# Performance work log

Hardware: AMD Instinct MI355X
Metric: run time of the kernel (lower is better)

The kernel has to match this reference:

```python
import jax, jax.numpy as jnp
import numpy as np

N_NODES = 100000
N_EDGES = 1600000
F_IN = 128
H = 32
N_CLASSES = 2
N_GRAPHS = 1000
BN_EPS = 1e-5


def _glorot(key, shape):
    fan_in, fan_out = shape
    lim = float(np.sqrt(6.0 / (fan_in + fan_out)))
    return jax.random.uniform(key, shape, jnp.float32, -lim, lim)


def setup_inputs() -> dict:
    key = jax.random.key(0)
    ks = jax.random.split(key, 16)
    x = jax.random.normal(ks[0], (N_NODES, F_IN), jnp.float32)
    edge_index = jax.random.randint(ks[1], (2, N_EDGES), 0, N_NODES, jnp.int64)
    batch = jnp.sort(jax.random.randint(ks[2], (N_NODES,), 0, N_GRAPHS, jnp.int64))
    return {
        "x": x,
        "edge_index": edge_index,
        "batch": batch,
        # GIN layer 1 MLP: Linear(F_IN,H) -> BN(H) -> ReLU -> Linear(H,H)
        "W1": _glorot(ks[3], (F_IN, H)), "b1": jnp.zeros((H,), jnp.float32),
        "g1": jnp.ones((H,), jnp.float32), "be1": jnp.zeros((H,), jnp.float32),
        "W2": _glorot(ks[4], (H, H)), "b2": jnp.zeros((H,), jnp.float32),
        # GIN layer 2 MLP
        "W3": _glorot(ks[5], (H, H)), "b3": jnp.zeros((H,), jnp.float32),
        "g2": jnp.ones((H,), jnp.float32), "be2": jnp.zeros((H,), jnp.float32),
        "W4": _glorot(ks[6], (H, H)), "b4": jnp.zeros((H,), jnp.float32),
        # classifier: Linear(2H,H) -> ReLU -> (Dropout eval) -> Linear(H,C)
        "Wc1": _glorot(ks[7], (2 * H, H)), "bc1": jnp.zeros((H,), jnp.float32),
        "Wc2": _glorot(ks[8], (H, N_CLASSES)), "bc2": jnp.zeros((N_CLASSES,), jnp.float32),
    }


def _gin_conv(x, src, dst, W_a, b_a, g, be, W_b, b_b):
    # GIN aggregation with eps=0: (1+eps)*x + sum_{j in N(i)} x_j
    agg = x + jax.ops.segment_sum(x[src], dst, num_segments=N_NODES)
    h = agg @ W_a + b_a                    # [N, H]
    # BatchNorm1d over node dim (training-mode batch stats)
    mu = jnp.mean(h, axis=0)
    var = jnp.var(h, axis=0)
    h = (h - mu) * jax.lax.rsqrt(var + BN_EPS) * g + be
    h = jax.nn.relu(h)
    return h @ W_b + b_b                   # [N, H]


def reference(x, edge_index, batch,
              W1, b1, g1, be1, W2, b2,
              W3, b3, g2, be2, W4, b4,
              Wc1, bc1, Wc2, bc2):
    src, dst = edge_index[0], edge_index[1]
    h = jax.nn.relu(_gin_conv(x, src, dst, W1, b1, g1, be1, W2, b2))
    h = _gin_conv(h, src, dst, W3, b3, g2, be2, W4, b4)   # [N, H]
    # global mean + max pool per graph
    counts = jax.ops.segment_sum(jnp.ones((N_NODES,), h.dtype), batch,
                                 num_segments=N_GRAPHS)              # [G]
    sums = jax.ops.segment_sum(h, batch, num_segments=N_GRAPHS)      # [G, H]
    mean = sums / jnp.maximum(counts, 1.0)[:, None]
    mx = jax.ops.segment_max(h, batch, num_segments=N_GRAPHS)
    mx = jnp.where(counts[:, None] > 0, mx, 0.0)
    z = jnp.concatenate([mean, mx], axis=-1)                          # [G, 2H]
    z = jax.nn.relu(z @ Wc1 + bc1)                                    # dropout: eval mode (identity)
    return z @ Wc2 + bc2                                              # [G, C]
```

## Files before the change

### kernel.cpp

```cpp
#include <hip/hip_runtime.h>


#define H 32
#define FIN 128
#define AGG_BLOCKS 2048
#define BNRED_NB 64

#define BKT_SHIFT 9
#define BKT_SZ 512
#define ACHUNK 4096

__device__ __forceinline__ int lower_bound_i(const int* __restrict__ a, int n, int key) {
  int lo = 0, hi = n;
  while (lo < hi) { int mid = (lo + hi) >> 1; if (a[mid] < key) lo = mid + 1; else hi = mid; }
  return lo;
}


__global__ __launch_bounds__(256) void k_bhist(const int* __restrict__ dst, int E,
                                               int* __restrict__ gbcnt) {
  __shared__ int cnt[256];
  int t = threadIdx.x;
  int e0 = blockIdx.x * ACHUNK, e1 = min(e0 + ACHUNK, E);
  cnt[t] = 0;
  __syncthreads();
  for (int i = e0 + t; i < e1; i += 256) atomicAdd(&cnt[dst[i] >> BKT_SHIFT], 1);
  __syncthreads();
  if (cnt[t] > 0) atomicAdd(&gbcnt[t], cnt[t]);
}

__global__ __launch_bounds__(256) void k_bscan(const int* __restrict__ gbcnt, int nbuck,
                                               int* __restrict__ bbase, int* __restrict__ bcur) {
  int t = threadIdx.x;
  __shared__ int sh[256];
  int v0 = (t < nbuck) ? gbcnt[t] : 0;
  sh[t] = v0;
  __syncthreads();
  for (int d = 1; d < 256; d <<= 1) {
    int v = (t >= d) ? sh[t - d] : 0;
    __syncthreads();
    sh[t] += v;
    __syncthreads();
  }
  int excl = sh[t] - v0;
  if (t < nbuck) { bbase[t] = excl; bcur[t] = excl; }
  if (t == 255) bbase[nbuck] = sh[255];
}

__global__ __launch_bounds__(256) void k_bucketA(const int* __restrict__ src, const int* __restrict__ dst,
                                                 int E, int* __restrict__ bcur,
                                                 unsigned* __restrict__ staging) {
  __shared__ int cnt[256];
  __shared__ int base[256];
  int t = threadIdx.x;
  int e0 = blockIdx.x * ACHUNK, e1 = min(e0 + ACHUNK, E);
  cnt[t] = 0;
  __syncthreads();
  for (int i = e0 + t; i < e1; i += 256) atomicAdd(&cnt[dst[i] >> BKT_SHIFT], 1);
  __syncthreads();
  int c = cnt[t];
  base[t] = (c > 0) ? atomicAdd(&bcur[t], c) : 0;
  __syncthreads();
  for (int i = e0 + t; i < e1; i += 256) {
    int d = dst[i];
    int p = atomicAdd(&base[d >> BKT_SHIFT], 1);
    staging[p] = ((unsigned)(d & (BKT_SZ - 1)) << 17) | (unsigned)src[i];
  }
}

__global__ __launch_bounds__(256) void k_bucketB(const unsigned* __restrict__ staging,
                                                 const int* __restrict__ bbase, int N,
                                                 int* __restrict__ row_ptr, int* __restrict__ csr) {
  __shared__ int cnt[BKT_SZ];
  __shared__ int ptr[BKT_SZ];
  __shared__ int sc[256];
  int t = threadIdx.x, b = blockIdx.x;
  int nb0 = b << BKT_SHIFT;
  int nb1 = min(nb0 + BKT_SZ, N);
  int seg0 = bbase[b];
  int len = bbase[b + 1] - seg0;
  cnt[t] = 0; cnt[t + 256] = 0;
  __syncthreads();
  for (int i = t; i < len; i += 256) atomicAdd(&cnt[staging[seg0 + i] >> 17], 1);
  __syncthreads();
  int s2 = cnt[2 * t] + cnt[2 * t + 1];
  sc[t] = s2;
  __syncthreads();
  for (int d = 1; d < 256; d <<= 1) {
    int v = (t >= d) ? sc[t - d] : 0;
    __syncthreads();
    sc[t] += v;
    __syncthreads();
  }
  int base0 = sc[t] - s2;
  ptr[2 * t] = base0;
  ptr[2 * t + 1] = base0 + cnt[2 * t];
  __syncthreads();
  int nn = nb1 - nb0;
  if (2 * t < nn)     row_ptr[nb0 + 2 * t]     = seg0 + ptr[2 * t];
  if (2 * t + 1 < nn) row_ptr[nb0 + 2 * t + 1] = seg0 + ptr[2 * t + 1];
  if (t == 0 && nb1 == N) row_ptr[N] = seg0 + len;
  __syncthreads();
  for (int i = t; i < len; i += 256) {
    unsigned e = staging[seg0 + i];
    int d = (int)(e >> 17);
    int k = atomicAdd(&ptr[d], 1);
    csr[seg0 + k] = (int)(e & 0x1FFFFu);
  }
}


__global__ __launch_bounds__(256) void k_gemm1(const float* __restrict__ x, const float* __restrict__ W,
                                               float* __restrict__ y, int N) {
  __shared__ __align__(16) float ws[FIN * H];
  __shared__ __align__(16) float xs[128 * 33];
  int t = threadIdx.x;
  for (int i = t; i < FIN * H; i += 256) ws[i] = W[i];
  int nb = blockIdx.x * 128;
  int r0 = (t >> 3) * 4;
  int c0 = (t & 7) * 4;
  float acc[4][4] = {{0.f,0.f,0.f,0.f},{0.f,0.f,0.f,0.f},{0.f,0.f,0.f,0.f},{0.f,0.f,0.f,0.f}};
  for (int kb = 0; kb < FIN; kb += 32) {
    __syncthreads();
    for (int i = t; i < 1024; i += 256) {
      int n = i >> 3, k4 = (i & 7) * 4;
      float4 v = make_float4(0.f, 0.f, 0.f, 0.f);
      int gn = nb + n;
      if (gn < N) v = *(const float4*)&x[(size_t)gn * FIN + kb + k4];
      xs[n * 33 + k4 + 0] = v.x; xs[n * 33 + k4 + 1] = v.y;
      xs[n * 33 + k4 + 2] = v.z; xs[n * 33 + k4 + 3] = v.w;
    }
    __syncthreads();
#pragma unroll
    for (int k = 0; k < 32; ++k) {
      float4 wv = *(const float4*)&ws[(kb + k) * H + c0];
      float x0 = xs[(r0 + 0) * 33 + k];
      float x1 = xs[(r0 + 1) * 33 + k];
      float x2 = xs[(r0 + 2) * 33 + k];
      float x3 = xs[(r0 + 3) * 33 + k];
      acc[0][0] += x0 * wv.x; acc[0][1] += x0 * wv.y; acc[0][2] += x0 * wv.z; acc[0][3] += x0 * wv.w;
      acc[1][0] += x1 * wv.x; acc[1][1] += x1 * wv.y; acc[1][2] += x1 * wv.z; acc[1][3] += x1 * wv.w;
      acc[2][0] += x2 * wv.x; acc[2][1] += x2 * wv.y; acc[2][2] += x2 * wv.z; acc[2][3] += x2 * wv.w;
      acc[3][0] += x3 * wv.x; acc[3][1] += x3 * wv.y; acc[3][2] += x3 * wv.z; acc[3][3] += x3 * wv.w;
    }
  }
#pragma unroll
  for (int r = 0; r < 4; ++r) {
    int gn = nb + r0 + r;
    if (gn < N)
      *(float4*)&y[(size_t)gn * H + c0] = make_float4(acc[r][0], acc[r][1], acc[r][2], acc[r][3]);
  }
}

__global__ __launch_bounds__(256) void k_agg(const float* __restrict__ y, const float* __restrict__ bias,
                                             const int* __restrict__ row_ptr, const int* __restrict__ csr,
                                             float* __restrict__ hout, float* __restrict__ bn_part, int N) {
  int wid = threadIdx.x >> 6, lane = threadIdx.x & 63;
  int c = lane & 31, ep = lane >> 5;
  float rsum = 0.f, rsq = 0.f;
  float bc = bias[c];
  int stride = gridDim.x * 4;
  for (int n = blockIdx.x * 4 + wid; n < N; n += stride) {
    int beg = row_ptr[n], end = row_ptr[n + 1];
    float acc = 0.f;
    for (int b0 = beg; b0 < end; b0 += 64) {
      int m = end - b0; if (m > 64) m = 64;
      int idx = (lane < m) ? csr[b0 + lane] : 0;
      int r = 0;
      for (; r + 8 <= m; r += 8) {
        int j0 = __shfl(idx, r + 0 + ep, 64);
        int j1 = __shfl(idx, r + 2 + ep, 64);
        int j2 = __shfl(idx, r + 4 + ep, 64);
        int j3 = __shfl(idx, r + 6 + ep, 64);
        float v0 = y[(size_t)j0 * H + c];
        float v1 = y[(size_t)j1 * H + c];
        float v2 = y[(size_t)j2 * H + c];
        float v3 = y[(size_t)j3 * H + c];
        acc += (v0 + v1) + (v2 + v3);
      }
      for (; r < m; r += 2) {
        int s = r + ep;
        int j = __shfl(idx, (s < m) ? s : 0, 64);
        float val = y[(size_t)j * H + c];
        if (s < m) acc += val;
      }
    }
    acc += __shfl_xor(acc, 32, 64);
    float v = acc + y[(size_t)n * H + c] + bc;
    if (ep == 0) {
      hout[(size_t)n * H + c] = v;
      rsum += v; rsq += v * v;
    }
  }
  __shared__ float bsum[4][H], bsq[4][H];
  if (ep == 0) { bsum[wid][c] = rsum; bsq[wid][c] = rsq; }
  __syncthreads();
  if (threadIdx.x < H) {
    int cc = threadIdx.x;
    bn_part[(size_t)blockIdx.x * 64 + cc]     = bsum[0][cc] + bsum[1][cc] + bsum[2][cc] + bsum[3][cc];
    bn_part[(size_t)blockIdx.x * 64 + H + cc] = bsq[0][cc] + bsq[1][cc] + bsq[2][cc] + bsq[3][cc];
  }
}

__global__ __launch_bounds__(256) void k_bnred(const float* __restrict__ part,
                                               float* __restrict__ part2) {
  int t = threadIdx.x, b = blockIdx.x;
  int col = t & 63, q = t >> 6;
  int rpb = AGG_BLOCKS / BNRED_NB;
  int r0 = b * rpb + q * (rpb / 4);
  float s = 0.f;
  for (int r = r0; r < r0 + rpb / 4; ++r) s += part[(size_t)r * 64 + col];
  __shared__ float red[4][64];
  red[q][col] = s;
  __syncthreads();
  if (t < 64) part2[(size_t)b * 64 + t] = red[0][t] + red[1][t] + red[2][t] + red[3][t];
}

__global__ __launch_bounds__(256) void k_bnfin(const float* __restrict__ part, int nblk,
                                               const float* __restrict__ gma, const float* __restrict__ bet,
                                               float* __restrict__ sc, float invN) {
  int t = threadIdx.x;
  int col = t & 63, q = t >> 6;
  int per = nblk >> 2;
  float s = 0.f;
  for (int r = q * per; r < (q + 1) * per; ++r) s += part[(size_t)r * 64 + col];
  __shared__ float red[4][64];
  __shared__ float tot[64];
  red[q][col] = s;
  __syncthreads();
  if (t < 64) tot[t] = red[0][t] + red[1][t] + red[2][t] + red[3][t];
  __syncthreads();
  if (t < H) {
    float mean = tot[t] * invN;
    float var = tot[H + t] * invN - mean * mean;
    float scale = gma[t] * rsqrtf(var + 1e-5f);
    sc[t] = scale;
    sc[H + t] = bet[t] - mean * scale;
  }
}

__global__ __launch_bounds__(256) void k_mlp1(const float* __restrict__ h1, const float* __restrict__ sc,
                                              const float* __restrict__ W2, const float* __restrict__ b2,
                                              const float* __restrict__ W3, float* __restrict__ y2, int N) {
  __shared__ __align__(16) float ws2[H * H], ws3[H * H];
  __shared__ __align__(16) float as[128 * 33];
  __shared__ __align__(16) float us[128 * 33];
  __shared__ float scs[2 * H], b2s[H];
  int t = threadIdx.x;
  for (int i = t; i < H * H; i += 256) { ws2[i] = W2[i]; ws3[i] = W3[i]; }
  if (t < 2 * H) scs[t] = sc[t];
  if (t < H) b2s[t] = b2[t];
  __syncthreads();
  int nb = blockIdx.x * 128;
  for (int i = t; i < 1024; i += 256) {
    int n = i >> 3, c4 = (i & 7) * 4;
    int gn = nb + n;
    float4 v = make_float4(0.f, 0.f, 0.f, 0.f);
    if (gn < N) v = *(const float4*)&h1[(size_t)gn * H + c4];
    as[n * 33 + c4 + 0] = fmaxf(v.x * scs[c4 + 0] + scs[H + c4 + 0], 0.f);
    as[n * 33 + c4 + 1] = fmaxf(v.y * scs[c4 + 1] + scs[H + c4 + 1], 0.f);
    as[n * 33 + c4 + 2] = fmaxf(v.z * scs[c4 + 2] + scs[H + c4 + 2], 0.f);
    as[n * 33 + c4 + 3] = fmaxf(v.w * scs[c4 + 3] + scs[H + c4 + 3], 0.f);
  }
  __syncthreads();
  int r0 = (t >> 3) * 4, c0 = (t & 7) * 4;
  float acc[4][4];
#pragma unroll
  for (int i = 0; i < 4; ++i)
#pragma unroll
    for (int j = 0; j < 4; ++j) acc[i][j] = b2s[c0 + j];
#pragma unroll
  for (int k = 0; k < H; ++k) {
    float4 wv = *(const float4*)&ws2[k * H + c0];
    float x0 = as[(r0 + 0) * 33 + k];
    float x1 = as[(r0 + 1) * 33 + k];
    float x2 = as[(r0 + 2) * 33 + k];
    float x3 = as[(r0 + 3) * 33 + k];
    acc[0][0] += x0 * wv.x; acc[0][1] += x0 * wv.y; acc[0][2] += x0 * wv.z; acc[0][3] += x0 * wv.w;
    acc[1][0] += x1 * wv.x; acc[1][1] += x1 * wv.y; acc[1][2] += x1 * wv.z; acc[1][3] += x1 * wv.w;
    acc[2][0] += x2 * wv.x; acc[2][1] += x2 * wv.y; acc[2][2] += x2 * wv.z; acc[2][3] += x2 * wv.w;
    acc[3][0] += x3 * wv.x; acc[3][1] += x3 * wv.y; acc[3][2] += x3 * wv.z; acc[3][3] += x3 * wv.w;
  }
#pragma unroll
  for (int i = 0; i < 4; ++i) {
    us[(r0 + i) * 33 + c0 + 0] = fmaxf(acc[i][0], 0.f);
    us[(r0 + i) * 33 + c0 + 1] = fmaxf(acc[i][1], 0.f);
    us[(r0 + i) * 33 + c0 + 2] = fmaxf(acc[i][2], 0.f);
    us[(r0 + i) * 33 + c0 + 3] = fmaxf(acc[i][3], 0.f);
  }
  __syncthreads();
#pragma unroll
  for (int i = 0; i < 4; ++i)
#pragma unroll
    for (int j = 0; j < 4; ++j) acc[i][j] = 0.f;
#pragma unroll
  for (int k = 0; k < H; ++k) {
    float4 wv = *(const float4*)&ws3[k * H + c0];
    float x0 = us[(r0 + 0) * 33 + k];
    float x1 = us[(r0 + 1) * 33 + k];
    float x2 = us[(r0 + 2) * 33 + k];
    float x3 = us[(r0 + 3) * 33 + k];
    acc[0][0] += x0 * wv.x; acc[0][1] += x0 * wv.y; acc[0][2] += x0 * wv.z; acc[0][3] += x0 * wv.w;
    acc[1][0] += x1 * wv.x; acc[1][1] += x1 * wv.y; acc[1][2] += x1 * wv.z; acc[1][3] += x1 * wv.w;
    acc[2][0] += x2 * wv.x; acc[2][1] += x2 * wv.y; acc[2][2] += x2 * wv.z; acc[2][3] += x2 * wv.w;
    acc[3][0] += x3 * wv.x; acc[3][1] += x3 * wv.y; acc[3][2] += x3 * wv.z; acc[3][3] += x3 * wv.w;
  }
#pragma unroll
  for (int i = 0; i < 4; ++i) {
    int gn = nb + r0 + i;
    if (gn < N)
      *(float4*)&y2[(size_t)gn * H + c0] = make_float4(acc[i][0], acc[i][1], acc[i][2], acc[i][3]);
  }
}

__global__ __launch_bounds__(256) void k_mlp2(const float* __restrict__ hpre, const float* __restrict__ sc,
                                              const float* __restrict__ W4, const float* __restrict__ b4,
                                              float* __restrict__ h2, int N) {
  __shared__ __align__(16) float ws4[H * H];
  __shared__ __align__(16) float as[128 * 33];
  __shared__ float scs[2 * H], b4s[H];
  int t = threadIdx.x;
  for (int i = t; i < H * H; i += 256) ws4[i] = W4[i];
  if (t < 2 * H) scs[t] = sc[t];
  if (t < H) b4s[t] = b4[t];
  __syncthreads();
  int nb = blockIdx.x * 128;
  for (int i = t; i < 1024; i += 256) {
    int n = i >> 3, c4 = (i & 7) * 4;
    int gn = nb + n;
    float4 v = make_float4(0.f, 0.f, 0.f, 0.f);
    if (gn < N) v = *(const float4*)&hpre[(size_t)gn * H + c4];
    as[n * 33 + c4 + 0] = fmaxf(v.x * scs[c4 + 0] + scs[H + c4 + 0], 0.f);
    as[n * 33 + c4 + 1] = fmaxf(v.y * scs[c4 + 1] + scs[H + c4 + 1], 0.f);
    as[n * 33 + c4 + 2] = fmaxf(v.z * scs[c4 + 2] + scs[H + c4 + 2], 0.f);
    as[n * 33 + c4 + 3] = fmaxf(v.w * scs[c4 + 3] + scs[H + c4 + 3], 0.f);
  }
  __syncthreads();
  int r0 = (t >> 3) * 4, c0 = (t & 7) * 4;
  float acc[4][4];
#pragma unroll
  for (int i = 0; i < 4; ++i)
#pragma unroll
    for (int j = 0; j < 4; ++j) acc[i][j] = b4s[c0 + j];
#pragma unroll
  for (int k = 0; k < H; ++k) {
    float4 wv = *(const float4*)&ws4[k * H + c0];
    float x0 = as[(r0 + 0) * 33 + k];
    float x1 = as[(r0 + 1) * 33 + k];
    float x2 = as[(r0 + 2) * 33 + k];
    float x3 = as[(r0 + 3) * 33 + k];
    acc[0][0] += x0 * wv.x; acc[0][1] += x0 * wv.y; acc[0][2] += x0 * wv.z; acc[0][3] += x0 * wv.w;
    acc[1][0] += x1 * wv.x; acc[1][1] += x1 * wv.y; acc[1][2] += x1 * wv.z; acc[1][3] += x1 * wv.w;
    acc[2][0] += x2 * wv.x; acc[2][1] += x2 * wv.y; acc[2][2] += x2 * wv.z; acc[2][3] += x2 * wv.w;
    acc[3][0] += x3 * wv.x; acc[3][1] += x3 * wv.y; acc[3][2] += x3 * wv.z; acc[3][3] += x3 * wv.w;
  }
#pragma unroll
  for (int i = 0; i < 4; ++i) {
    int gn = nb + r0 + i;
    if (gn < N)
      *(float4*)&h2[(size_t)gn * H + c0] = make_float4(acc[i][0], acc[i][1], acc[i][2], acc[i][3]);
  }
}

__global__ __launch_bounds__(256) void k_pool(const float* __restrict__ h2, const int* __restrict__ batch,
                                              int N, int G, float* __restrict__ z) {
  int wid = threadIdx.x >> 6, lane = threadIdx.x & 63;
  int g = blockIdx.x * 4 + wid;
  if (g >= G) return;
  int beg = lower_bound_i(batch, N, g);
  int end = lower_bound_i(batch, N, g + 1);
  int c = lane & 31, ep = lane >> 5;
  float s = 0.f, m = -3.402823466e38f;
  for (int i = beg + ep; i < end; i += 2) {
    float v = h2[(size_t)i * H + c];
    s += v; m = fmaxf(m, v);
  }
  s += __shfl_xor(s, 32, 64);
  m = fmaxf(m, __shfl_xor(m, 32, 64));
  if (ep == 0) {
    int cnt = end - beg;
    z[(size_t)g * 64 + c]     = (cnt > 0) ? s / (float)cnt : 0.f;
    z[(size_t)g * 64 + H + c] = (cnt > 0) ? m : 0.f;
  }
}

__global__ __launch_bounds__(256) void k_cls(const float* __restrict__ z, const float* __restrict__ Wc1,
                                             const float* __restrict__ bc1, const float* __restrict__ Wc2,
                                             const float* __restrict__ bc2, float* __restrict__ out, int G) {
  __shared__ __align__(16) float w1s[64 * H];
  __shared__ float w2s[H * 2], b1s[H], b2s[2];
  int t = threadIdx.x;
  for (int i = t; i < 64 * H; i += 256) w1s[i] = Wc1[i];
  if (t < H * 2) w2s[t] = Wc2[t];
  if (t < H) b1s[t] = bc1[t];
  if (t < 2) b2s[t] = bc2[t];
  __syncthreads();
  int g = blockIdx.x * 256 + t;
  if (g >= G) return;
  float zr[64], u[H];
  const float4* zp = (const float4*)&z[(size_t)g * 64];
#pragma unroll
  for (int q = 0; q < 16; ++q) {
    float4 v = zp[q];
    zr[q * 4 + 0] = v.x; zr[q * 4 + 1] = v.y; zr[q * 4 + 2] = v.z; zr[q * 4 + 3] = v.w;
  }
#pragma unroll
  for (int c = 0; c < H; ++c) u[c] = b1s[c];
#pragma unroll
  for (int k = 0; k < 64; ++k) {
    float av = zr[k];
    const float4* wr = (const float4*)&w1s[k * H];
#pragma unroll
    for (int q = 0; q < H / 4; ++q) {
      float4 wv = wr[q];
      u[q * 4 + 0] += av * wv.x; u[q * 4 + 1] += av * wv.y;
      u[q * 4 + 2] += av * wv.z; u[q * 4 + 3] += av * wv.w;
    }
  }
  float o0 = b2s[0], o1 = b2s[1];
#pragma unroll
  for (int k = 0; k < H; ++k) {
    float uv = fmaxf(u[k], 0.f);
    o0 += uv * w2s[k * 2 + 0];
    o1 += uv * w2s[k * 2 + 1];
  }
  out[(size_t)g * 2 + 0] = o0;
  out[(size_t)g * 2 + 1] = o1;
}

extern "C" void kernel_launch(void* const* d_in, const int* in_sizes, int n_in,
                              void* d_out, int out_size, void* d_ws, size_t ws_size,
                              hipStream_t stream) {
  const float* x    = (const float*)d_in[0];
  const int*   eidx = (const int*)d_in[1];
  const int*   batch= (const int*)d_in[2];
  const float* W1 = (const float*)d_in[3];
  const float* b1 = (const float*)d_in[4];
  const float* g1 = (const float*)d_in[5];
  const float* be1= (const float*)d_in[6];
  const float* W2 = (const float*)d_in[7];
  const float* b2 = (const float*)d_in[8];
  const float* W3 = (const float*)d_in[9];
  const float* b3 = (const float*)d_in[10];
  const float* g2 = (const float*)d_in[11];
  const float* be2= (const float*)d_in[12];
  const float* W4 = (const float*)d_in[13];
  const float* b4 = (const float*)d_in[14];
  const float* Wc1= (const float*)d_in[15];
  const float* bc1= (const float*)d_in[16];
  const float* Wc2= (const float*)d_in[17];
  const float* bc2= (const float*)d_in[18];
  (void)n_in; (void)ws_size;

  int N = in_sizes[2];
  int E = in_sizes[1] / 2;
  int G = out_size / 2;
  int nbuck = (N + BKT_SZ - 1) >> BKT_SHIFT;
  const int* srcv = eidx;
  const int* dstv = eidx + E;

  char* w = (char*)d_ws;
  auto carve = [&](size_t bytes) { void* p = (void*)w; w += (bytes + 255) & ~(size_t)255; return p; };
  float*    bufA    = (float*)carve((size_t)N * H * 4);
  float*    bufB    = (float*)carve((size_t)N * H * 4);
  int*      row_ptr = (int*)carve((size_t)(N + 1) * 4);
  int*      csr     = (int*)carve((size_t)E * 4);
  unsigned* staging = (unsigned*)carve((size_t)E * 4);
  int*      gbcnt   = (int*)carve(256 * 4);
  int*      bbase   = (int*)carve(257 * 4);
  int*      bcur    = (int*)carve(256 * 4);
  float*    bnp     = (float*)carve((size_t)AGG_BLOCKS * 64 * 4);
  float*    bnp2    = (float*)carve((size_t)BNRED_NB * 64 * 4);
  float*    sc1     = (float*)carve(64 * 4);
  float*    sc2     = (float*)carve(64 * 4);
  float*    z       = (float*)carve((size_t)G * 64 * 4);

  int abk = (E + ACHUNK - 1) / ACHUNK;
  int tblk = (N + 127) / 128;

  hipMemsetAsync(gbcnt, 0, 256 * 4, stream);
  k_bhist<<<abk, 256, 0, stream>>>(dstv, E, gbcnt);
  k_bscan<<<1, 256, 0, stream>>>(gbcnt, nbuck, bbase, bcur);
  k_bucketA<<<abk, 256, 0, stream>>>(srcv, dstv, E, bcur, staging);
  k_bucketB<<<nbuck, 256, 0, stream>>>(staging, bbase, N, row_ptr, csr);
  k_gemm1<<<tblk, 256, 0, stream>>>(x, W1, bufA, N);
  k_agg<<<AGG_BLOCKS, 256, 0, stream>>>(bufA, b1, row_ptr, csr, bufB, bnp, N);
  k_bnred<<<BNRED_NB, 256, 0, stream>>>(bnp, bnp2);
  k_bnfin<<<1, 256, 0, stream>>>(bnp2, BNRED_NB, g1, be1, sc1, 1.0f / (float)N);
  k_mlp1<<<tblk, 256, 0, stream>>>(bufB, sc1, W2, b2, W3, bufA, N);
  k_agg<<<AGG_BLOCKS, 256, 0, stream>>>(bufA, b3, row_ptr, csr, bufB, bnp, N);
  k_bnred<<<BNRED_NB, 256, 0, stream>>>(bnp, bnp2);
  k_bnfin<<<1, 256, 0, stream>>>(bnp2, BNRED_NB, g2, be2, sc2, 1.0f / (float)N);
  k_mlp2<<<tblk, 256, 0, stream>>>(bufB, sc2, W4, b4, bufA, N);
  k_pool<<<(G + 3) / 4, 256, 0, stream>>>(bufA, batch, N, G, z);
  k_cls<<<(G + 255) / 256, 256, 0, stream>>>(z, Wc1, bc1, Wc2, bc2, (float*)d_out, G);
}
```

Before: 389.6 us.

## Double-buffer x tiles in gemm1 with register prefetch and smaller row tiles

Rewrites the first GEMM so each block handles 64 rows instead of 128, doubling the block count. The x tile goes into two shared-memory buffers, and the next K-slice is prefetched into registers while the current one is computed. This hides global load latency and removes one barrier per iteration. In exchange each block still loads the full 16 KB W tile, so W traffic and setup per row double, and each thread computes 2x4 outputs instead of 4x4.

```diff
diff --git a/kernel.cpp b/kernel.cpp
--- a/kernel.cpp
+++ b/kernel.cpp
@@ -5,6 +5,7 @@
 #define FIN 128
 #define AGG_BLOCKS 2048
 #define BNRED_NB 64
+#define G1R 64
 
 #define BKT_SHIFT 9
 #define BKT_SZ 512
@@ -113,40 +114,53 @@
 __global__ __launch_bounds__(256) void k_gemm1(const float* __restrict__ x, const float* __restrict__ W,
                                                float* __restrict__ y, int N) {
   __shared__ __align__(16) float ws[FIN * H];
-  __shared__ __align__(16) float xs[128 * 33];
+  __shared__ __align__(16) float xs[2][G1R * 33];
   int t = threadIdx.x;
   for (int i = t; i < FIN * H; i += 256) ws[i] = W[i];
-  int nb = blockIdx.x * 128;
-  int r0 = (t >> 3) * 4;
-  int c0 = (t & 7) * 4;
-  float acc[4][4] = {{0.f,0.f,0.f,0.f},{0.f,0.f,0.f,0.f},{0.f,0.f,0.f,0.f},{0.f,0.f,0.f,0.f}};
+  int nb = blockIdx.x * G1R;
+  int n0 = t >> 3,            k40 = (t & 7) * 4;
+  int n1 = (t + 256) >> 3,    k41 = (t & 7) * 4;
+  const float4* xr0 = (nb + n0 < N) ? (const float4*)&x[(size_t)(nb + n0) * FIN] : nullptr;
+  const float4* xr1 = (nb + n1 < N) ? (const float4*)&x[(size_t)(nb + n1) * FIN] : nullptr;
+  float4 p0 = make_float4(0.f, 0.f, 0.f, 0.f), p1 = p0;
+  if (xr0) p0 = xr0[k40 >> 2];
+  if (xr1) p1 = xr1[k41 >> 2];
+  xs[0][n0 * 33 + k40 + 0] = p0.x; xs[0][n0 * 33 + k40 + 1] = p0.y;
+  xs[0][n0 * 33 + k40 + 2] = p0.z; xs[0][n0 * 33 + k40 + 3] = p0.w;
+  xs[0][n1 * 33 + k41 + 0] = p1.x; xs[0][n1 * 33 + k41 + 1] = p1.y;
+  xs[0][n1 * 33 + k41 + 2] = p1.z; xs[0][n1 * 33 + k41 + 3] = p1.w;
+  __syncthreads();
+  int rr = (t >> 3) * 2, c0 = (t & 7) * 4;
+  float acc[2][4] = {{0.f,0.f,0.f,0.f},{0.f,0.f,0.f,0.f}};
   for (int kb = 0; kb < FIN; kb += 32) {
-    __syncthreads();
-    for (int i = t; i < 1024; i += 256) {
-      int n = i >> 3, k4 = (i & 7) * 4;
-      float4 v = make_float4(0.f, 0.f, 0.f, 0.f);
-      int gn = nb + n;
-      if (gn < N) v = *(const float4*)&x[(size_t)gn * FIN + kb + k4];
-      xs[n * 33 + k4 + 0] = v.x; xs[n * 33 + k4 + 1] = v.y;
-      xs[n * 33 + k4 + 2] = v.z; xs[n * 33 + k4 + 3] = v.w;
+    int cur = (kb >> 5) & 1;
+    bool more = (kb + 32) < FIN;
+    if (more) {
+      p0 = make_float4(0.f, 0.f, 0.f, 0.f); p1 = p0;
+      int kq = (kb + 32 + k40) >> 2;
+      if (xr0) p0 = xr0[kq];
+      if (xr1) p1 = xr1[kq];
+    }
+#pragma unroll
+    for (int k = 0; k < 32; ++k) {
+      float4 wv = *(const float4*)&ws[(kb + k) * H + c0];
+      float x0 = xs[cur][(rr + 0) * 33 + k];
+      float x1 = xs[cur][(rr + 1) * 33 + k];
+      acc[0][0] += x0 * wv.x; acc[0][1] += x0 * wv.y; acc[0][2] += x0 * wv.z; acc[0][3] += x0 * wv.w;
+      acc[1][0] += x1 * wv.x; acc[1][1] += x1 * wv.y; acc[1][2] += x1 * wv.z; acc[1][3] += x1 * wv.w;
+    }
+    if (more) {
+      int nx = cur ^ 1;
+      xs[nx][n0 * 33 + k40 + 0] = p0.x; xs[nx][n0 * 33 + k40 + 1] = p0.y;
+      xs[nx][n0 * 33 + k40 + 2] = p0.z; xs[nx][n0 * 33 + k40 + 3] = p0.w;
+      xs[nx][n1 * 33 + k41 + 0] = p1.x; xs[nx][n1 * 33 + k41 + 1] = p1.y;
+      xs[nx][n1 * 33 + k41 + 2] = p1.z; xs[nx][n1 * 33 + k41 + 3] = p1.w;
     }
     __syncthreads();
-#pragma unroll
-    for (int k = 0; k < 32; ++k) {
-      float4 wv = *(const float4*)&ws[(kb + k) * H + c0];
-      float x0 = xs[(r0 + 0) * 33 + k];
-      float x1 = xs[(r0 + 1) * 33 + k];
-      float x2 = xs[(r0 + 2) * 33 + k];
-      float x3 = xs[(r0 + 3) * 33 + k];
-      acc[0][0] += x0 * wv.x; acc[0][1] += x0 * wv.y; acc[0][2] += x0 * wv.z; acc[0][3] += x0 * wv.w;
-      acc[1][0] += x1 * wv.x; acc[1][1] += x1 * wv.y; acc[1][2] += x1 * wv.z; acc[1][3] += x1 * wv.w;
-      acc[2][0] += x2 * wv.x; acc[2][1] += x2 * wv.y; acc[2][2] += x2 * wv.z; acc[2][3] += x2 * wv.w;
-      acc[3][0] += x3 * wv.x; acc[3][1] += x3 * wv.y; acc[3][2] += x3 * wv.z; acc[3][3] += x3 * wv.w;
-    }
-  }
-#pragma unroll
-  for (int r = 0; r < 4; ++r) {
-    int gn = nb + r0 + r;
+  }
+#pragma unroll
+  for (int r = 0; r < 2; ++r) {
+    int gn = nb + rr + r;
     if (gn < N)
       *(float4*)&y[(size_t)gn * H + c0] = make_float4(acc[r][0], acc[r][1], acc[r][2], acc[r][3]);
   }
@@ -476,6 +490,7 @@
   float*    z       = (float*)carve((size_t)G * 64 * 4);
 
   int abk = (E + ACHUNK - 1) / ACHUNK;
+  int g1blk = (N + G1R - 1) / G1R;
   int tblk = (N + 127) / 128;
 
   hipMemsetAsync(gbcnt, 0, 256 * 4, stream);
@@ -483,7 +498,7 @@
   k_bscan<<<1, 256, 0, stream>>>(gbcnt, nbuck, bbase, bcur);
   k_bucketA<<<abk, 256, 0, stream>>>(srcv, dstv, E, bcur, staging);
   k_bucketB<<<nbuck, 256, 0, stream>>>(staging, bbase, N, row_ptr, csr);
-  k_gemm1<<<tblk, 256, 0, stream>>>(x, W1, bufA, N);
+  k_gemm1<<<g1blk, 256, 0, stream>>>(x, W1, bufA, N);
   k_agg<<<AGG_BLOCKS, 256, 0, stream>>>(bufA, b1, row_ptr, csr, bufB, bnp, N);
   k_bnred<<<BNRED_NB, 256, 0, stream>>>(bnp, bnp2);
   k_bnfin<<<1, 256, 0, stream>>>(bnp2, BNRED_NB, g1, be1, sc1, 1.0f / (float)N);
```

New measurement: 680.9 us. 74.8% more time.
